# Optimization experiments

Measured on AMD Instinct MI355X. Metric: run time of the kernel, lower is better.

## Reference

```python
import jax, jax.numpy as jnp
import numpy as np

E, H, F, N, B = 512, 8, 2048, 1024, 4
HD = E // H


def setup_inputs() -> dict:
    key = jax.random.key(0)
    ks = jax.random.split(key, 20)
    s = 0.02
    return {
        "node_inputs": jax.random.normal(ks[0], (N, B, E), jnp.float32),
        "parent_mask": jax.random.uniform(ks[1], (B, N, N), jnp.float32),
        "hidden": jax.random.bernoulli(ks[2], 0.5, (B, N, N)),
        "pad_mask": jax.random.bernoulli(ks[3], 0.1, (B, N)),
        "Wp": jax.random.normal(ks[4], (H, E), jnp.float32) * s,
        "bp": jnp.zeros((H,), jnp.float32),
        "Wc": jax.random.normal(ks[5], (H, E), jnp.float32) * s,
        "bc": jnp.zeros((H,), jnp.float32),
        "Wqkv": jax.random.normal(ks[6], (3 * E, E), jnp.float32) * s,
        "bqkv": jnp.zeros((3 * E,), jnp.float32),
        "Wo": jax.random.normal(ks[7], (E, E), jnp.float32) * s,
        "bo": jnp.zeros((E,), jnp.float32),
        "W1": jax.random.normal(ks[8], (F, E), jnp.float32) * s,
        "b1": jnp.zeros((F,), jnp.float32),
        "W2": jax.random.normal(ks[9], (E, F), jnp.float32) * s,
        "b2": jnp.zeros((E,), jnp.float32),
        "ln1_g": jnp.ones((E,), jnp.float32),
        "ln1_b": jnp.zeros((E,), jnp.float32),
        "ln2_g": jnp.ones((E,), jnp.float32),
        "ln2_b": jnp.zeros((E,), jnp.float32),
    }


def _layer_norm(x, g, b, eps=1e-5):
    m = jnp.mean(x, axis=-1, keepdims=True)
    v = jnp.mean((x - m) ** 2, axis=-1, keepdims=True)
    return (x - m) * jax.lax.rsqrt(v + eps) * g + b


def reference(node_inputs, parent_mask, hidden, pad_mask, Wp, bp, Wc, bc,
              Wqkv, bqkv, Wo, bo, W1, b1, W2, b2, ln1_g, ln1_b, ln2_g, ln2_b):
    x = node_inputs  # (N, B, E), seq-first like nn.TransformerEncoderLayer
    # parent/child per-head biases: Linear(E->H), permuted to (B, H, N)
    pbias = jnp.transpose(x @ Wp.T + bp, (1, 2, 0))
    cbias = jnp.transpose(x @ Wc.T + bc, (1, 2, 0))
    # additive attention bias (B, H, N, N)
    am = (jnp.swapaxes(parent_mask, 1, 2)[:, None] * pbias[..., None]
          + parent_mask[:, None] * cbias[..., None])
    am = jnp.where(hidden[:, None], -jnp.inf, am)
    # multi-head self-attention
    qkv = x @ Wqkv.T + bqkv  # (N, B, 3E)
    q, k, v = jnp.split(qkv, 3, axis=-1)

    def heads(t):  # (N, B, E) -> (B, H, N, HD)
        return jnp.transpose(t.reshape(N, B, H, HD), (1, 2, 0, 3))

    q, k, v = heads(q), heads(k), heads(v)
    scores = jnp.einsum("bhqd,bhkd->bhqk", q, k) / jnp.sqrt(jnp.float32(HD)) + am
    scores = jnp.where(pad_mask[:, None, None, :], -jnp.inf, scores)
    attn = jax.nn.softmax(scores, axis=-1)
    ctx = jnp.einsum("bhqk,bhkd->bhqd", attn, v)  # (B, H, N, HD)
    ctx = jnp.transpose(ctx, (2, 0, 1, 3)).reshape(N, B, E)
    attn_out = ctx @ Wo.T + bo
    # post-norm transformer encoder layer (dropout=0, relu activation)
    y = _layer_norm(x + attn_out, ln1_g, ln1_b)
    ff = jax.nn.relu(y @ W1.T + b1) @ W2.T + b2
    return _layer_norm(y + ff, ln2_g, ln2_b)
```

## Files before the change

### kernel.cpp

```cpp
#include <hip/hip_runtime.h>
#include <hip/hip_bf16.h>
#include <stdint.h>

using bf16 = __hip_bfloat16;

typedef __bf16 bf16x8 __attribute__((ext_vector_type(8)));
typedef float  f32x4  __attribute__((ext_vector_type(4)));

__device__ __forceinline__ float bflo(uint32_t u) { return __uint_as_float(u << 16); }
__device__ __forceinline__ float bfhi(uint32_t u) { return __uint_as_float(u & 0xffff0000u); }

__device__ __forceinline__ void load8(const bf16* p, float* f) {
  uint4 u = *(const uint4*)p;
  f[0] = bflo(u.x); f[1] = bfhi(u.x);
  f[2] = bflo(u.y); f[3] = bfhi(u.y);
  f[4] = bflo(u.z); f[5] = bfhi(u.z);
  f[6] = bflo(u.w); f[7] = bfhi(u.w);
}
__device__ __forceinline__ void load8(const float* p, float* f) {
  float4 a = *(const float4*)p, b = *(const float4*)(p + 4);
  f[0] = a.x; f[1] = a.y; f[2] = a.z; f[3] = a.w;
  f[4] = b.x; f[5] = b.y; f[6] = b.z; f[7] = b.w;
}
__device__ __forceinline__ void store1(float* o, float v) { *o = v; }
__device__ __forceinline__ void store1(bf16* o, float v) { *o = __float2bfloat16(v); }
__device__ __forceinline__ uint32_t bfbits(float x) {
  bf16 v = __float2bfloat16(x);
  return (uint32_t)*(uint16_t*)&v;
}

typedef const uint32_t __attribute__((address_space(1)))* gp_t;
typedef uint32_t __attribute__((address_space(3)))* lp_t;
__device__ __forceinline__ void gload16(const void* g, void* l) {
  __builtin_amdgcn_global_load_lds((gp_t)g, (lp_t)l, 16, 0, 0);
}

__global__ __launch_bounds__(256)
void cvt_prep(const float* __restrict__ x, const float* __restrict__ Wqkv,
              const float* __restrict__ Wo, const float* __restrict__ W1,
              const float* __restrict__ W2, bf16* __restrict__ xb,
              bf16* __restrict__ wq, bf16* __restrict__ wob,
              bf16* __restrict__ w1b, bf16* __restrict__ w2b,
              const float* __restrict__ bqkv, const float* __restrict__ bp,
              const float* __restrict__ bc, const float* __restrict__ Wp,
              const float* __restrict__ Wc, float* __restrict__ bias_ext)
{
  const int blk = blockIdx.x, t = threadIdx.x;
  if (blk < 2560) {
    size_t j = ((size_t)blk * 256 + t) * 8;
    const float* s; bf16* o; size_t off;
    if      (j < 2097152) { s = x;    o = xb;  off = j; }
    else if (j < 2883584) { s = Wqkv; o = wq;  off = j - 2097152; }
    else if (j < 3145728) { s = Wo;   o = wob; off = j - 2883584; }
    else if (j < 4194304) { s = W1;   o = w1b; off = j - 3145728; }
    else                  { s = W2;   o = w2b; off = j - 4194304; }
    float f[8];
    load8(s + off, f);
    uint4 u;
    u.x = (bfbits(f[1]) << 16) | bfbits(f[0]);
    u.y = (bfbits(f[3]) << 16) | bfbits(f[2]);
    u.z = (bfbits(f[5]) << 16) | bfbits(f[4]);
    u.w = (bfbits(f[7]) << 16) | bfbits(f[6]);
    *(uint4*)(o + off) = u;
  } else {
    int sb = blk - 2560;
    if (sb < 2) {
      int j = (sb * 256 + t) * 8;
      if (j < 4096) {
        float f[8]; load8(Wp + j, f);
#pragma unroll
        for (int i = 0; i < 8; ++i) wq[(size_t)1536 * 512 + j + i] = __float2bfloat16(f[i]);
      }
    } else if (sb < 4) {
      int j = ((sb - 2) * 256 + t) * 8;
      if (j < 4096) {
        float f[8]; load8(Wc + j, f);
#pragma unroll
        for (int i = 0; i < 8; ++i) wq[(size_t)1544 * 512 + j + i] = __float2bfloat16(f[i]);
      }
    } else {
      int j = t * 8;
#pragma unroll
      for (int i = 0; i < 8; ++i) {
        int cc = j + i;
        if (cc < 1664) {
          float v = 0.f;
          if (cc < 1536) v = bqkv[cc];
          else if (cc < 1544) v = bp[cc - 1536];
          else if (cc < 1552) v = bc[cc - 1544];
          bias_ext[cc] = v;
        }
      }
    }
  }
}

__global__ __launch_bounds__(256)
void mask_pack(const float* __restrict__ pm, const int* __restrict__ hid,
               const int* __restrict__ padm, uint32_t* __restrict__ mout)
{
  __shared__ float tileT[128][65];
  const int t = threadIdx.x, mb = blockIdx.x;
  const int k0 = (mb & 7) * 128, q0 = ((mb >> 3) & 15) * 64, b = mb >> 7;
  const size_t pb = (size_t)b << 20;
#pragma unroll
  for (int i = 0; i < 32; ++i) {
    int idx = t + i * 256;
    int r = idx >> 6, c = idx & 63;
    tileT[r][c] = pm[pb + (size_t)(k0 + r) * 1024 + q0 + c];
  }
  __syncthreads();
#pragma unroll
  for (int i = 0; i < 32; ++i) {
    int idx = t + i * 256;
    int q = idx >> 7, k = idx & 127;
    size_t src = pb + (size_t)(q0 + q) * 1024 + k0 + k;
    int msk = hid[src] | padm[b * 1024 + k0 + k];
    uint32_t u = 0xFFFFFFFFu;
    if (!msk) u = (bfbits(tileT[k][q]) << 16) | bfbits(pm[src]);
    mout[src] = u;
  }
}

__global__ __launch_bounds__(256)
void qkv_gemm(const bf16* __restrict__ A, const bf16* __restrict__ W,
              const float* __restrict__ bias, bf16* __restrict__ outb,
              float* __restrict__ outf)
{
  __shared__ bf16 As[2][128 * 64];
  __shared__ bf16 Bs[2][128 * 64];
  const int t = threadIdx.x;
  const int lane = t & 63, wave = t >> 6;
  const int m0 = (blockIdx.x / 13) * 128, n0 = (blockIdx.x % 13) * 128;
  const int wr = wave >> 1, wc = wave & 1;
  const int frow = lane & 15, ksel = (lane >> 4) * 8;
  f32x4 acc[16] = {};
  const bf16* Ab = A + (size_t)m0 * 512;
  const bf16* Wb = W + (size_t)n0 * 512;

  const int ibs = wave * 64 + lane;
#define STAGE(buf, k0)                                                        \
  {                                                                           \
    _Pragma("unroll")                                                         \
    for (int i = 0; i < 4; ++i) {                                             \
      int idx = i * 256 + ibs;                                                \
      gload16(Ab + (size_t)(idx >> 3) * 512 + (k0) + (idx & 7) * 8,           \
              &As[buf][(i * 256 + wave * 64) * 8]);                           \
    }                                                                         \
    _Pragma("unroll")                                                         \
    for (int i = 0; i < 4; ++i) {                                             \
      int idx = i * 256 + ibs;                                                \
      gload16(Wb + (size_t)(idx >> 3) * 512 + (k0) + (idx & 7) * 8,           \
              &Bs[buf][(i * 256 + wave * 64) * 8]);                           \
    }                                                                         \
  }

  STAGE(0, 0);
  __syncthreads();
#pragma unroll
  for (int ks = 0; ks < 8; ++ks) {
    const int cur = ks & 1;
    if (ks < 7) STAGE(cur ^ 1, (ks + 1) * 64);
#pragma unroll
    for (int kk = 0; kk < 64; kk += 32) {
      bf16x8 af[4], bf_[4];
#pragma unroll
      for (int mt = 0; mt < 4; ++mt)
        af[mt] = *(const bf16x8*)(&As[cur][(wr * 64 + mt * 16 + frow) * 64 + kk + ksel]);
#pragma unroll
      for (int nt = 0; nt < 4; ++nt)
        bf_[nt] = *(const bf16x8*)(&Bs[cur][(wc * 64 + nt * 16 + frow) * 64 + kk + ksel]);
#pragma unroll
      for (int mt = 0; mt < 4; ++mt)
#pragma unroll
        for (int nt = 0; nt < 4; ++nt)
          acc[mt * 4 + nt] = __builtin_amdgcn_mfma_f32_16x16x32_bf16(
              af[mt], bf_[nt], acc[mt * 4 + nt], 0, 0, 0);
    }
    __syncthreads();
  }
#undef STAGE

  const int rb = (lane >> 4) * 4, cb = lane & 15;
#pragma unroll
  for (int mt = 0; mt < 4; ++mt)
#pragma unroll
    for (int nt = 0; nt < 4; ++nt) {
      f32x4 a = acc[mt * 4 + nt];
#pragma unroll
      for (int r = 0; r < 4; ++r) {
        int row = m0 + wr * 64 + mt * 16 + rb + r;
        int col = n0 + wc * 64 + nt * 16 + cb;
        if (col >= 1552) continue;
        float v = a[r] + bias[col];
        int n = row >> 2, b = row & 3;
        if (col >= 1536) {
          int j = col - 1536;
          int hh = j & 7;
          outf[(j < 8 ? 0 : 32768) + (b * 8 + hh) * 1024 + n] = v;
        } else {
          int which = col >> 9, hh = (col >> 6) & 7, d = col & 63;
          if (which == 0) v *= 0.125f;
          size_t idx;
          if (which == 2)
            idx = (((size_t)(64 + b * 8 + hh)) << 16) + (size_t)d * 1024 + n;
          else
            idx = (((size_t)(which * 32 + b * 8 + hh)) << 16) + (size_t)n * 64 + d;
          outb[idx] = __float2bfloat16(v);
        }
      }
    }
}

template<int MODE, int BN>
__global__ __launch_bounds__(256)
void gemm_bt(const bf16* __restrict__ A, const bf16* __restrict__ W,
             const float* __restrict__ bias, bf16* __restrict__ outb,
             float* __restrict__ outf, int M, int Nout, int K, int kLen)
{
  constexpr int NT = BN / 32;
  __shared__ bf16 As[128 * 64];
  __shared__ bf16 Bs[BN * 64];
  const int t = threadIdx.x, lane = t & 63, wave = t >> 6;
  const int m0 = blockIdx.y * 128, n0 = blockIdx.x * BN;
  const int kOff = blockIdx.z * kLen;
  if (MODE == 3) outf += (size_t)blockIdx.z * M * Nout;
  const int wr = wave >> 1, wc = wave & 1;
  const int frow = lane & 15, ksel = (lane >> 4) * 8;
  f32x4 acc[4 * NT] = {};
  const bf16* Ab = A + (size_t)m0 * K;
  const bf16* Wb = W + (size_t)n0 * K;

  for (int k0 = kOff; k0 < kOff + kLen; k0 += 64) {
    __syncthreads();
#pragma unroll
    for (int i = 0; i < 4; ++i) {
      int ib = i * 256 + wave * 64;
      int idx = ib + lane;
      gload16(Ab + (size_t)(idx >> 3) * K + k0 + (idx & 7) * 8, As + ib * 8);
    }
#pragma unroll
    for (int i = 0; i < BN / 32; ++i) {
      int ib = i * 256 + wave * 64;
      int idx = ib + lane;
      gload16(Wb + (size_t)(idx >> 3) * K + k0 + (idx & 7) * 8, Bs + ib * 8);
    }
    __syncthreads();
#pragma unroll
    for (int kk = 0; kk < 64; kk += 32) {
      bf16x8 af[4], bf_[NT];
#pragma unroll
      for (int mt = 0; mt < 4; ++mt)
        af[mt] = *(const bf16x8*)(As + (wr * 64 + mt * 16 + frow) * 64 + kk + ksel);
#pragma unroll
      for (int nt = 0; nt < NT; ++nt)
        bf_[nt] = *(const bf16x8*)(Bs + (wc * (BN / 2) + nt * 16 + frow) * 64 + kk + ksel);
#pragma unroll
      for (int mt = 0; mt < 4; ++mt)
#pragma unroll
        for (int nt = 0; nt < NT; ++nt)
          acc[mt * NT + nt] = __builtin_amdgcn_mfma_f32_16x16x32_bf16(
              af[mt], bf_[nt], acc[mt * NT + nt], 0, 0, 0);
    }
  }
  const int rb = (lane >> 4) * 4, cb = lane & 15;
#pragma unroll
  for (int mt = 0; mt < 4; ++mt)
#pragma unroll
    for (int nt = 0; nt < NT; ++nt) {
      f32x4 a = acc[mt * NT + nt];
#pragma unroll
      for (int r = 0; r < 4; ++r) {
        int row = m0 + wr * 64 + mt * 16 + rb + r;
        int col = n0 + wc * (BN / 2) + nt * 16 + cb;
        if (MODE == 3) {
          outf[(size_t)row * Nout + col] = a[r];
        } else {
          float v = a[r] + bias[col];
          if (MODE == 1) v = fmaxf(v, 0.f);
          outb[(size_t)row * Nout + col] = __float2bfloat16(v);
        }
      }
    }
}

__global__ __launch_bounds__(256, 3)
void attn_mfma(const bf16* __restrict__ qkv, const float* __restrict__ pbw,
               const float* __restrict__ cbw, const uint32_t* __restrict__ mpk,
               bf16* __restrict__ opart, float2* __restrict__ mlout)
{
  __shared__ bf16 Kt[128 * 64];
  __shared__ bf16 Vt[64 * 128];
  __shared__ bf16 Ps[4][16][136];
  const int t = threadIdx.x, lane = t & 63, wave = t >> 6;
  const int g = lane >> 4, c = lane & 15;
  const int h = blockIdx.y, b = blockIdx.z >> 1, half = blockIdx.z & 1;
  const int q0 = blockIdx.x * 64 + wave * 16;
  const size_t bh = (size_t)b * 8 + h;
  const bf16* Qp = qkv + (bh << 16);
  const bf16* Kp = qkv + ((32 + bh) << 16);
  const bf16* Vg = qkv + ((64 + bh) << 16);

  bf16x8 qa0 = *(const bf16x8*)(Qp + (size_t)(q0 + c) * 64 + g * 8);
  bf16x8 qa1 = *(const bf16x8*)(Qp + (size_t)(q0 + c) * 64 + 32 + g * 8);

  const float pbq = pbw[bh * 1024 + q0 + c];
  const float cbq = cbw[bh * 1024 + q0 + c];
  const uint32_t* mrp = mpk + (((size_t)b * 1024 + q0 + c) << 10);

  f32x4 oacc[4] = {{0,0,0,0},{0,0,0,0},{0,0,0,0},{0,0,0,0}};
  float m = -1e30f, l = 0.f;

  for (int kt = 0; kt < 4; ++kt) {
    const int k0 = half * 512 + kt * 128;
    __syncthreads();
#pragma unroll
    for (int i = 0; i < 4; ++i) {
      int ib = i * 256 + wave * 64;
      int idx = ib + lane;
      int r = idx >> 3, p = idx & 7;
      gload16(Kp + (size_t)(k0 + r) * 64 + ((p ^ (r & 7)) * 8), Kt + ib * 8);
    }
#pragma unroll
    for (int i = 0; i < 4; ++i) {
      int ib = i * 256 + wave * 64;
      int idx = ib + lane;
      int d = idx >> 4, p = idx & 15;
      gload16(Vg + (size_t)d * 1024 + k0 + ((p ^ (d & 15)) * 8), Vt + ib * 8);
    }
    uint4 mu[8];
#pragma unroll
    for (int nt = 0; nt < 8; ++nt)
      mu[nt] = *(const uint4*)(mrp + k0 + nt * 16 + 4 * g);
    __syncthreads();
    f32x4 sacc[8];
#pragma unroll
    for (int nt = 0; nt < 8; ++nt) {
      f32x4 z = {0.f,0.f,0.f,0.f};
      int r = nt * 16 + c;
      bf16x8 k0f = *(const bf16x8*)(Kt + r * 64 + (( g      ^ (c & 7)) * 8));
      bf16x8 k1f = *(const bf16x8*)(Kt + r * 64 + (((4 + g) ^ (c & 7)) * 8));
      z = __builtin_amdgcn_mfma_f32_16x16x32_bf16(k0f, qa0, z, 0, 0, 0);
      z = __builtin_amdgcn_mfma_f32_16x16x32_bf16(k1f, qa1, z, 0, 0, 0);
      sacc[nt] = z;
    }
    float mx = -1e30f;
#pragma unroll
    for (int nt = 0; nt < 8; ++nt) {
      uint32_t uu[4] = {mu[nt].x, mu[nt].y, mu[nt].z, mu[nt].w};
#pragma unroll
      for (int r = 0; r < 4; ++r) {
        float s = sacc[nt][r] + bfhi(uu[r]) * pbq + bflo(uu[r]) * cbq;
        s = (uu[r] == 0xFFFFFFFFu) ? -1e30f : s;
        sacc[nt][r] = s;
        mx = fmaxf(mx, s);
      }
    }
    mx = fmaxf(mx, __shfl_xor(mx, 16));
    mx = fmaxf(mx, __shfl_xor(mx, 32));
    const float newm = fmaxf(m, mx);
    const float al = __expf(m - newm);
    float ps = 0.f;
#pragma unroll
    for (int nt = 0; nt < 8; ++nt) {
      float p0 = (sacc[nt][0] <= -1e29f) ? 0.f : __expf(sacc[nt][0] - newm);
      float p1 = (sacc[nt][1] <= -1e29f) ? 0.f : __expf(sacc[nt][1] - newm);
      float p2 = (sacc[nt][2] <= -1e29f) ? 0.f : __expf(sacc[nt][2] - newm);
      float p3 = (sacc[nt][3] <= -1e29f) ? 0.f : __expf(sacc[nt][3] - newm);
      ps += (p0 + p1) + (p2 + p3);
      uint2 w;
      w.x = (bfbits(p1) << 16) | bfbits(p0);
      w.y = (bfbits(p3) << 16) | bfbits(p2);
      *(uint2*)&Ps[wave][c][nt * 16 + 4 * g] = w;
    }
    ps += __shfl_xor(ps, 16);
    ps += __shfl_xor(ps, 32);
    l = l * al + ps;
    m = newm;
#pragma unroll
    for (int dt = 0; dt < 4; ++dt) {
      oacc[dt][0] *= al; oacc[dt][1] *= al;
      oacc[dt][2] *= al; oacc[dt][3] *= al;
    }
#pragma unroll
    for (int dt = 0; dt < 4; ++dt) {
      int row = dt * 16 + c;
#pragma unroll
      for (int kc = 0; kc < 4; ++kc) {
        bf16x8 vf = *(const bf16x8*)(Vt + row * 128 + (((kc * 4 + g) ^ c) * 8));
        bf16x8 pf = *(const bf16x8*)&Ps[wave][c][kc * 32 + g * 8];
        oacc[dt] = __builtin_amdgcn_mfma_f32_16x16x32_bf16(vf, pf, oacc[dt], 0, 0, 0);
      }
    }
  }
  const int qg = q0 + c;
  const size_t prow = ((size_t)(half * 32) + bh) * 1024 + qg;
#pragma unroll
  for (int dt = 0; dt < 4; ++dt)
#pragma unroll
    for (int rg = 0; rg < 4; ++rg)
      opart[prow * 64 + dt * 16 + 4 * g + rg] = __float2bfloat16(oacc[dt][rg]);
  if (g == 0) mlout[prow] = make_float2(m, l);
}

__global__ __launch_bounds__(256)
void attn_reduce(const bf16* __restrict__ opart, const float2* __restrict__ ml,
                 bf16* __restrict__ ctxo)
{
  const int idx = blockIdx.x * 256 + threadIdx.x;
  const int row = idx >> 3, seg = (idx & 7) * 8;
  float o0[8], o1[8];
  load8(opart + (size_t)row * 64 + seg, o0);
  load8(opart + (size_t)(row + 32768) * 64 + seg, o1);
  const float2 ml0 = ml[row], ml1 = ml[row + 32768];
  const float mst = fmaxf(ml0.x, ml1.x);
  const float w0 = __expf(ml0.x - mst), w1 = __expf(ml1.x - mst);
  const float denom = ml0.y * w0 + ml1.y * w1;
  const float inv = (denom > 0.f) ? 1.f / denom : 0.f;
  const int bh = row >> 10, q = row & 1023;
  const int b = bh >> 3, h = bh & 7;
  bf16* out = ctxo + ((size_t)q * 4 + b) * 512 + h * 64 + seg;
#pragma unroll
  for (int j = 0; j < 8; ++j)
    out[j] = __float2bfloat16((o0[j] * w0 + o1[j] * w1) * inv);
}

template<typename TA, typename TO>
__global__ __launch_bounds__(256)
void ln_res2(const TA* __restrict__ a, const float* __restrict__ p0,
             const float* __restrict__ p1, const float* __restrict__ bias,
             const float* __restrict__ g, const float* __restrict__ be,
             TO* __restrict__ out)
{
  const int wave = threadIdx.x >> 6, lane = threadIdx.x & 63;
  const int m = blockIdx.x * 4 + wave;
  const size_t base = (size_t)m * 512 + lane * 8;
  float va[8], f0[8], f1[8], bb[8];
  load8(a + base, va);
  load8(p0 + base, f0);
  load8(p1 + base, f1);
  load8(bias + lane * 8, bb);
  float v[8], s = 0.f;
#pragma unroll
  for (int j = 0; j < 8; ++j) { v[j] = va[j] + f0[j] + f1[j] + bb[j]; s += v[j]; }
#pragma unroll
  for (int off = 32; off; off >>= 1) s += __shfl_xor(s, off);
  const float mean = s * (1.f / 512.f);
  float q = 0.f;
#pragma unroll
  for (int j = 0; j < 8; ++j) { float d = v[j] - mean; q += d * d; }
#pragma unroll
  for (int off = 32; off; off >>= 1) q += __shfl_xor(q, off);
  const float rs = rsqrtf(q * (1.f / 512.f) + 1e-5f);
  float gv[8], bv[8];
  load8(g + lane * 8, gv);
  load8(be + lane * 8, bv);
#pragma unroll
  for (int j = 0; j < 8; ++j)
    store1(out + base + j, (v[j] - mean) * rs * gv[j] + bv[j]);
}

extern "C" void kernel_launch(void* const* d_in, const int* in_sizes, int n_in,
                              void* d_out, int out_size, void* d_ws, size_t ws_size,
                              hipStream_t stream)
{
  (void)in_sizes; (void)n_in; (void)out_size; (void)ws_size;
  const float* x    = (const float*)d_in[0];
  const float* pm   = (const float*)d_in[1];
  const int*   hid  = (const int*)d_in[2];
  const int*   padm = (const int*)d_in[3];
  const float* Wp   = (const float*)d_in[4];
  const float* bp   = (const float*)d_in[5];
  const float* Wc   = (const float*)d_in[6];
  const float* bc   = (const float*)d_in[7];
  const float* Wqkv = (const float*)d_in[8];
  const float* bqkv = (const float*)d_in[9];
  const float* Wo   = (const float*)d_in[10];
  const float* bo   = (const float*)d_in[11];
  const float* W1   = (const float*)d_in[12];
  const float* b1   = (const float*)d_in[13];
  const float* W2   = (const float*)d_in[14];
  const float* b2   = (const float*)d_in[15];
  const float* g1   = (const float*)d_in[16];
  const float* be1  = (const float*)d_in[17];
  const float* g2   = (const float*)d_in[18];
  const float* be2  = (const float*)d_in[19];

  char* ws = (char*)d_ws;
  bf16*     qkvb  = (bf16*)    (ws);
  float*    pbo   = (float*)   (ws + 12582912);
  float*    cbo   = (float*)   (ws + 12713984);
  uint32_t* mpk   = (uint32_t*)(ws + 12845056);
  bf16*     ctx   = (bf16*)    (ws + 29622272);
  float*    part  = (float*)   (ws);
  bf16*     ff1   = (bf16*)    (ws + 16777216);
  bf16*     y     = (bf16*)    (ws + 33816576);
  bf16*     xb    = (bf16*)    (ws + 38010880);
  bf16*     wqkvb = (bf16*)    (ws + 42205184);
  bf16*     wob   = (bf16*)    (ws + 43909120);
  bf16*     w1b   = (bf16*)    (ws + 44433408);
  bf16*     w2b   = (bf16*)    (ws + 46530560);
  float*    bext  = (float*)   (ws + 48627712);
  bf16*     opart = (bf16*)    (ws + 48634368);
  float2*   mlb   = (float2*)  (ws + 57022976);
  float*    part1 = part + (size_t)4096 * 512;

  cvt_prep<<<2565, 256, 0, stream>>>(x, Wqkv, Wo, W1, W2, xb, wqkvb, wob, w1b, w2b,
                                     bqkv, bp, bc, Wp, Wc, bext);
  mask_pack<<<512, 256, 0, stream>>>(pm, hid, padm, mpk);
  qkv_gemm<<<416, 256, 0, stream>>>(xb, wqkvb, bext, qkvb, pbo);
  attn_mfma<<<dim3(16, 8, 8), 256, 0, stream>>>(qkvb, pbo, cbo, mpk, opart, mlb);
  attn_reduce<<<1024, 256, 0, stream>>>(opart, mlb, ctx);
  gemm_bt<3, 64><<<dim3(8, 32, 2), 256, 0, stream>>>(ctx, wob, nullptr, nullptr, part, 4096, 512, 512, 256);
  ln_res2<float, bf16><<<1024, 256, 0, stream>>>(x, part, part1, bo, g1, be1, y);
  gemm_bt<1, 128><<<dim3(16, 32), 256, 0, stream>>>(y, w1b, b1, ff1, nullptr, 4096, 2048, 512, 512);
  gemm_bt<3, 64><<<dim3(8, 32, 2), 256, 0, stream>>>(ff1, w2b, nullptr, nullptr, part, 4096, 512, 2048, 1024);
  ln_res2<bf16, float><<<1024, 256, 0, stream>>>(y, part, part1, b2, g2, be2, (float*)d_out);
}
```

Measured before the change: 276.0 us.

## Drop attention KV split and fuse mask packing into conversion prep kernel

The attention kernel now processes all 1024 keys per block instead of splitting them into two halves. It normalizes the output in-kernel and writes ctx directly, which removes the partial-output buffers and the separate reduce kernel. The mask packing and the fp32-to-bf16 conversion kernels are merged into one launch. Together this removes two launches and the partial-result traffic, but halves the attention grid to 512 blocks, and the occupancy hint drops from 3 to 2 blocks per CU, reducing parallelism in the attention stage.

```diff
diff --git a/kernel.cpp b/kernel.cpp
--- a/kernel.cpp
+++ b/kernel.cpp
@@ -36,16 +36,43 @@
 }
 
 __global__ __launch_bounds__(256)
-void cvt_prep(const float* __restrict__ x, const float* __restrict__ Wqkv,
-              const float* __restrict__ Wo, const float* __restrict__ W1,
-              const float* __restrict__ W2, bf16* __restrict__ xb,
-              bf16* __restrict__ wq, bf16* __restrict__ wob,
-              bf16* __restrict__ w1b, bf16* __restrict__ w2b,
-              const float* __restrict__ bqkv, const float* __restrict__ bp,
-              const float* __restrict__ bc, const float* __restrict__ Wp,
-              const float* __restrict__ Wc, float* __restrict__ bias_ext)
-{
-  const int blk = blockIdx.x, t = threadIdx.x;
+void prep_mask(const float* __restrict__ pm, const int* __restrict__ hid,
+               const int* __restrict__ padm, uint32_t* __restrict__ mout,
+               const float* __restrict__ x, const float* __restrict__ Wqkv,
+               const float* __restrict__ Wo, const float* __restrict__ W1,
+               const float* __restrict__ W2, bf16* __restrict__ xb,
+               bf16* __restrict__ wq, bf16* __restrict__ wob,
+               bf16* __restrict__ w1b, bf16* __restrict__ w2b,
+               const float* __restrict__ bqkv, const float* __restrict__ bp,
+               const float* __restrict__ bc, const float* __restrict__ Wp,
+               const float* __restrict__ Wc, float* __restrict__ bias_ext)
+{
+  __shared__ float tileT[128][65];
+  const int t = threadIdx.x;
+  if (blockIdx.x < 512) {
+    const int mb = blockIdx.x;
+    const int k0 = (mb & 7) * 128, q0 = ((mb >> 3) & 15) * 64, b = mb >> 7;
+    const size_t pb = (size_t)b << 20;
+#pragma unroll
+    for (int i = 0; i < 32; ++i) {
+      int idx = t + i * 256;
+      int r = idx >> 6, c = idx & 63;
+      tileT[r][c] = pm[pb + (size_t)(k0 + r) * 1024 + q0 + c];
+    }
+    __syncthreads();
+#pragma unroll
+    for (int i = 0; i < 32; ++i) {
+      int idx = t + i * 256;
+      int q = idx >> 7, k = idx & 127;
+      size_t src = pb + (size_t)(q0 + q) * 1024 + k0 + k;
+      int msk = hid[src] | padm[b * 1024 + k0 + k];
+      uint32_t u = 0xFFFFFFFFu;
+      if (!msk) u = (bfbits(tileT[k][q]) << 16) | bfbits(pm[src]);
+      mout[src] = u;
+    }
+    return;
+  }
+  const int blk = blockIdx.x - 512;
   if (blk < 2560) {
     size_t j = ((size_t)blk * 256 + t) * 8;
     const float* s; bf16* o; size_t off;
@@ -96,33 +123,6 @@
 }
 
 __global__ __launch_bounds__(256)
-void mask_pack(const float* __restrict__ pm, const int* __restrict__ hid,
-               const int* __restrict__ padm, uint32_t* __restrict__ mout)
-{
-  __shared__ float tileT[128][65];
-  const int t = threadIdx.x, mb = blockIdx.x;
-  const int k0 = (mb & 7) * 128, q0 = ((mb >> 3) & 15) * 64, b = mb >> 7;
-  const size_t pb = (size_t)b << 20;
-#pragma unroll
-  for (int i = 0; i < 32; ++i) {
-    int idx = t + i * 256;
-    int r = idx >> 6, c = idx & 63;
-    tileT[r][c] = pm[pb + (size_t)(k0 + r) * 1024 + q0 + c];
-  }
-  __syncthreads();
-#pragma unroll
-  for (int i = 0; i < 32; ++i) {
-    int idx = t + i * 256;
-    int q = idx >> 7, k = idx & 127;
-    size_t src = pb + (size_t)(q0 + q) * 1024 + k0 + k;
-    int msk = hid[src] | padm[b * 1024 + k0 + k];
-    uint32_t u = 0xFFFFFFFFu;
-    if (!msk) u = (bfbits(tileT[k][q]) << 16) | bfbits(pm[src]);
-    mout[src] = u;
-  }
-}
-
-__global__ __launch_bounds__(256)
 void qkv_gemm(const bf16* __restrict__ A, const bf16* __restrict__ W,
               const float* __restrict__ bias, bf16* __restrict__ outb,
               float* __restrict__ outf)
@@ -284,17 +284,17 @@
     }
 }
 
-__global__ __launch_bounds__(256, 3)
+__global__ __launch_bounds__(256, 2)
 void attn_mfma(const bf16* __restrict__ qkv, const float* __restrict__ pbw,
                const float* __restrict__ cbw, const uint32_t* __restrict__ mpk,
-               bf16* __restrict__ opart, float2* __restrict__ mlout)
+               bf16* __restrict__ ctxo)
 {
   __shared__ bf16 Kt[128 * 64];
   __shared__ bf16 Vt[64 * 128];
   __shared__ bf16 Ps[4][16][136];
   const int t = threadIdx.x, lane = t & 63, wave = t >> 6;
   const int g = lane >> 4, c = lane & 15;
-  const int h = blockIdx.y, b = blockIdx.z >> 1, half = blockIdx.z & 1;
+  const int h = blockIdx.y, b = blockIdx.z;
   const int q0 = blockIdx.x * 64 + wave * 16;
   const size_t bh = (size_t)b * 8 + h;
   const bf16* Qp = qkv + (bh << 16);
@@ -311,8 +311,8 @@
   f32x4 oacc[4] = {{0,0,0,0},{0,0,0,0},{0,0,0,0},{0,0,0,0}};
   float m = -1e30f, l = 0.f;
 
-  for (int kt = 0; kt < 4; ++kt) {
-    const int k0 = half * 512 + kt * 128;
+  for (int kt = 0; kt < 8; ++kt) {
+    const int k0 = kt * 128;
     __syncthreads();
 #pragma unroll
     for (int i = 0; i < 4; ++i) {
@@ -394,35 +394,15 @@
     }
   }
   const int qg = q0 + c;
-  const size_t prow = ((size_t)(half * 32) + bh) * 1024 + qg;
-#pragma unroll
-  for (int dt = 0; dt < 4; ++dt)
-#pragma unroll
-    for (int rg = 0; rg < 4; ++rg)
-      opart[prow * 64 + dt * 16 + 4 * g + rg] = __float2bfloat16(oacc[dt][rg]);
-  if (g == 0) mlout[prow] = make_float2(m, l);
-}
-
-__global__ __launch_bounds__(256)
-void attn_reduce(const bf16* __restrict__ opart, const float2* __restrict__ ml,
-                 bf16* __restrict__ ctxo)
-{
-  const int idx = blockIdx.x * 256 + threadIdx.x;
-  const int row = idx >> 3, seg = (idx & 7) * 8;
-  float o0[8], o1[8];
-  load8(opart + (size_t)row * 64 + seg, o0);
-  load8(opart + (size_t)(row + 32768) * 64 + seg, o1);
-  const float2 ml0 = ml[row], ml1 = ml[row + 32768];
-  const float mst = fmaxf(ml0.x, ml1.x);
-  const float w0 = __expf(ml0.x - mst), w1 = __expf(ml1.x - mst);
-  const float denom = ml0.y * w0 + ml1.y * w1;
-  const float inv = (denom > 0.f) ? 1.f / denom : 0.f;
-  const int bh = row >> 10, q = row & 1023;
-  const int b = bh >> 3, h = bh & 7;
-  bf16* out = ctxo + ((size_t)q * 4 + b) * 512 + h * 64 + seg;
-#pragma unroll
-  for (int j = 0; j < 8; ++j)
-    out[j] = __float2bfloat16((o0[j] * w0 + o1[j] * w1) * inv);
+  const float inv = (l > 0.f) ? 1.f / l : 0.f;
+  bf16* out = ctxo + ((size_t)qg * 4 + b) * 512 + h * 64;
+#pragma unroll
+  for (int dt = 0; dt < 4; ++dt) {
+    uint2 w;
+    w.x = (bfbits(oacc[dt][1] * inv) << 16) | bfbits(oacc[dt][0] * inv);
+    w.y = (bfbits(oacc[dt][3] * inv) << 16) | bfbits(oacc[dt][2] * inv);
+    *(uint2*)(out + dt * 16 + 4 * g) = w;
+  }
 }
 
 template<typename TA, typename TO>
@@ -501,16 +481,13 @@
   bf16*     w1b   = (bf16*)    (ws + 44433408);
   bf16*     w2b   = (bf16*)    (ws + 46530560);
   float*    bext  = (float*)   (ws + 48627712);
-  bf16*     opart = (bf16*)    (ws + 48634368);
-  float2*   mlb   = (float2*)  (ws + 57022976);
   float*    part1 = part + (size_t)4096 * 512;
 
-  cvt_prep<<<2565, 256, 0, stream>>>(x, Wqkv, Wo, W1, W2, xb, wqkvb, wob, w1b, w2b,
-                                     bqkv, bp, bc, Wp, Wc, bext);
-  mask_pack<<<512, 256, 0, stream>>>(pm, hid, padm, mpk);
+  prep_mask<<<3077, 256, 0, stream>>>(pm, hid, padm, mpk,
+                                      x, Wqkv, Wo, W1, W2, xb, wqkvb, wob, w1b, w2b,
+                                      bqkv, bp, bc, Wp, Wc, bext);
   qkv_gemm<<<416, 256, 0, stream>>>(xb, wqkvb, bext, qkvb, pbo);
-  attn_mfma<<<dim3(16, 8, 8), 256, 0, stream>>>(qkvb, pbo, cbo, mpk, opart, mlb);
-  attn_reduce<<<1024, 256, 0, stream>>>(opart, mlb, ctx);
+  attn_mfma<<<dim3(16, 8, 4), 256, 0, stream>>>(qkvb, pbo, cbo, mpk, ctx);
   gemm_bt<3, 64><<<dim3(8, 32, 2), 256, 0, stream>>>(ctx, wob, nullptr, nullptr, part, 4096, 512, 512, 256);
   ln_res2<float, bf16><<<1024, 256, 0, stream>>>(x, part, part1, bo, g1, be1, y);
   gemm_bt<1, 128><<<dim3(16, 32), 256, 0, stream>>>(y, w1b, b1, ff1, nullptr, 4096, 2048, 512, 512);
```

Result: faster. 258.7 us (-6.2%).
